# Kernel optimization log

Hardware: AMD Instinct MI355X
Metric: run time of the kernel (lower is better)

## Reference

```python
import jax, jax.numpy as jnp
import numpy as np

N = 100_000      # nodes
E = 1_600_000    # edges (avg degree 16)
D = 128          # emb_dim
L = 2            # num_layer
BN_EPS = 1e-5


def setup_inputs() -> dict:
    key = jax.random.key(0)
    ks = jax.random.split(key, 16)
    s = 0.05
    inp = {
        # int inputs
        "x": jax.random.randint(ks[0], (N, 9), 0, 2),
        "z": jax.random.randint(ks[1], (N,), 0, 1000),
        "edge_index": jax.random.randint(ks[2], (2, E), 0, N),
        "edge_attr": jax.random.randint(ks[3], (E, 3), 0, 2),
        # learned params
        "atom_emb": jax.random.normal(ks[4], (9, 119, D), jnp.float32) * s,  # padded stacked AtomEncoder tables
        "z_emb": jax.random.normal(ks[5], (1000, D), jnp.float32) * s,
        "bond_emb": jax.random.normal(ks[6], (L, 3, 6, D), jnp.float32) * s,  # padded BondEncoder tables per layer
        "eps": jnp.zeros((L,), jnp.float32),
        "W1": jax.random.normal(ks[7], (L, D, 2 * D), jnp.float32) * s,
        "b1": jnp.zeros((L, 2 * D), jnp.float32),
        "g1": jnp.ones((L, 2 * D), jnp.float32),
        "be1": jnp.zeros((L, 2 * D), jnp.float32),
        "W2": jax.random.normal(ks[8], (L, 2 * D, D), jnp.float32) * s,
        "b2": jnp.zeros((L, D), jnp.float32),
        "bng": jnp.ones((L, D), jnp.float32),
        "bnb": jnp.zeros((L, D), jnp.float32),
    }
    return inp


def _batchnorm(h, g, b):
    # training-mode BatchNorm1d: batch stats, biased variance
    m = h.mean(axis=0)
    v = h.var(axis=0)
    return (h - m) * jax.lax.rsqrt(v + BN_EPS) * g + b


def _multi_embed(tables, idx):
    # tables: [F, V, D], idx: [N, F] -> sum_f tables[f][idx[:, f]]  -> [N, D]
    return jax.vmap(lambda t, i: t[i], in_axes=(0, 1))(tables, idx).sum(axis=0)


def reference(x, z, edge_index, edge_attr, atom_emb, z_emb, bond_emb, eps,
              W1, b1, g1, be1, W2, b2, bng, bnb):
    src, dst = edge_index[0], edge_index[1]
    # h0 = AtomEncoder(x) + z_embedding(z)
    h = _multi_embed(atom_emb, x) + z_emb[z]
    for l in range(L):
        # GINConv: bond encode -> gather -> relu message -> scatter-add -> MLP
        e_emb = _multi_embed(bond_emb[l], edge_attr)          # [E, D]
        msg = jax.nn.relu(h[src] + e_emb)                      # [E, D]
        agg = jax.ops.segment_sum(msg, dst, num_segments=N)    # [N, D]
        pre = (1.0 + eps[l]) * h + agg
        hid = jax.nn.relu(_batchnorm(pre @ W1[l] + b1[l], g1[l], be1[l]))
        hconv = hid @ W2[l] + b2[l]
        h = _batchnorm(hconv, bng[l], bnb[l])
        if l < L - 1:
            h = jax.nn.relu(h)   # dropout ratio 0 -> identity
    return h
```

## Files before the change

kernel.cpp:

```cpp
#include <hip/hip_runtime.h>

#define D 128
#define BN_EPS 1e-5f
#define NSUB 1024
#define CAP2 2048

typedef __attribute__((ext_vector_type(8))) short short8;
typedef __attribute__((ext_vector_type(4))) float floatx4;

__device__ __forceinline__ float bf2f(unsigned short u) {
    unsigned int x = ((unsigned int)u) << 16;
    return __builtin_bit_cast(float, x);
}
__device__ __forceinline__ unsigned short f2bf(float f) {
    unsigned int x = __builtin_bit_cast(unsigned int, f);
    x = x + 0x7FFFu + ((x >> 16) & 1u);
    return (unsigned short)(x >> 16);
}
__device__ __forceinline__ int magdiv(unsigned int x, unsigned long long magic) {
    return (int)(((unsigned long long)x * magic) >> 44);
}

__global__ __launch_bounds__(256)
void setup_kernel(const int* __restrict__ x, const int* __restrict__ z,
                  const float* __restrict__ atom_emb, const float* __restrict__ z_emb,
                  unsigned short* __restrict__ hb, int N, int nbNode,
                  const float* __restrict__ bond_emb, float* __restrict__ comb,
                  const float* __restrict__ W1, unsigned short* __restrict__ w1p,
                  const float* __restrict__ W2, unsigned short* __restrict__ w2p) {
    const int b = blockIdx.x;
    const int tid = threadIdx.x;
    if (b < nbNode) {
        int gid = b * 256 + tid;
        int node = gid >> 5;
        if (node >= N) return;
        int d0 = (gid & 31) * 4;
        float4 acc = *(const float4*)(z_emb + (size_t)z[node] * D + d0);
#pragma unroll
        for (int f = 0; f < 9; ++f) {
            int v = x[node * 9 + f];
            const float4 t = *(const float4*)(atom_emb + (size_t)(f * 119 + v) * D + d0);
            acc.x += t.x; acc.y += t.y; acc.z += t.z; acc.w += t.w;
        }
        ushort4 o;
        o.x = f2bf(acc.x); o.y = f2bf(acc.y); o.z = f2bf(acc.z); o.w = f2bf(acc.w);
        *(ushort4*)(hb + (size_t)node * D + d0) = o;
    } else if (b < nbNode + 216) {
        int t = (b - nbNode) * 256 + tid;
        int layer = t / (216 * D);
        int idx = t - layer * (216 * D);
        int c = idx >> 7, d = idx & 127;
        int a0 = c / 36, a1 = (c / 6) % 6, a2 = c % 6;
        const float* bb = bond_emb + (size_t)layer * 3 * 6 * D;
        float v = bb[(0 * 6 + a0) * D + d] + bb[(1 * 6 + a1) * D + d] + bb[(2 * 6 + a2) * D + d];
        comb[(size_t)layer * 216 * D + idx] = v;
    } else {
        int isW2 = (b >= nbNode + 216 + 256);
        int t = (b - nbNode - 216 - (isW2 ? 256 : 0)) * 256 + tid;
        int layer = t >> 15;
        int idx = t & 32767;
        int logN = isW2 ? 7 : 8;
        int NCOLS = 1 << logN;
        int k = idx >> logN, n = idx & (NCOLS - 1);
        int k0 = k >> 5, kq = k & 31, q = kq >> 3, j = kq & 7;
        int tt = n >> 4, ln = n & 15;
        size_t dest = (((size_t)k0 * (NCOLS >> 4) + tt) << 9) + ((q << 4) + ln) * 8 + j;
        const float* W = (isW2 ? W2 : W1) + (size_t)layer * 32768;
        unsigned short* Wp = (isW2 ? w2p : w1p) + (size_t)layer * 32768;
        Wp[dest] = f2bf(W[idx]);
    }
}

__global__ __launch_bounds__(256)
void partition_kernel(const int* __restrict__ ei, const int* __restrict__ ea,
                      unsigned int* __restrict__ subL, int* __restrict__ tail2,
                      int E, int N, unsigned long long magic, int ntiles, int nblocks) {
    __shared__ int lcnt[1024], lbase[1024];
    const int tid = threadIdx.x;
    for (int tile = blockIdx.x; tile < ntiles; tile += nblocks) {
        const int tb = tile * 4096;
#pragma unroll
        for (int i = 0; i < 4; ++i) lcnt[tid + i * 256] = 0;
        __syncthreads();
        int sub[16];
        unsigned int entry[16];
#pragma unroll
        for (int j = 0; j < 16; ++j) {
            int e = tb + j * 256 + tid;
            if (e < E) {
                int dst = ei[E + e];
                int c = (ea[3 * e] * 6 + ea[3 * e + 1]) * 6 + ea[3 * e + 2];
                int k = magdiv((unsigned)dst * 1024u, magic);
                int lo = (int)(((long long)k * N + 1023) >> 10);
                sub[j] = k;
                entry[j] = (unsigned int)ei[e] | ((unsigned int)c << 17) |
                           ((unsigned int)(dst - lo) << 25);
                atomicAdd(&lcnt[k], 1);
            } else {
                sub[j] = -1;
            }
        }
        __syncthreads();
#pragma unroll
        for (int i = 0; i < 4; ++i) {
            int k = tid + i * 256;
            int c = lcnt[k];
            if (c) lbase[k] = atomicAdd(&tail2[k], c);
            lcnt[k] = 0;
        }
        __syncthreads();
#pragma unroll
        for (int j = 0; j < 16; ++j) {
            if (sub[j] >= 0) {
                int k = sub[j];
                int pos = lbase[k] + atomicAdd(&lcnt[k], 1);
                if (pos < CAP2) subL[(size_t)k * CAP2 + pos] = entry[j];
            }
        }
        __syncthreads();
    }
}

__global__ __launch_bounds__(1024)
void subscan_kernel(const int* __restrict__ tail2, int* __restrict__ subbase,
                    int* __restrict__ offsets, int N) {
    const int tid = threadIdx.x, lane = tid & 63, wid = tid >> 6;
    int v = min(tail2[tid], CAP2);
    int s = v;
#pragma unroll
    for (int off = 1; off < 64; off <<= 1) {
        int t = __shfl_up(s, off, 64);
        if (lane >= off) s += t;
    }
    __shared__ int ws[16];
    if (lane == 63) ws[wid] = s;
    __syncthreads();
    if (wid == 0) {
        int w = (lane < 16) ? ws[lane] : 0;
#pragma unroll
        for (int off = 1; off < 16; off <<= 1) {
            int t = __shfl_up(w, off, 64);
            if (lane >= off) w += t;
        }
        if (lane < 16) ws[lane] = w;
    }
    __syncthreads();
    int excl = (wid ? ws[wid - 1] : 0) + s - v;
    subbase[tid] = excl;
    if (tid == 1023) offsets[N] = excl + v;
}

__global__ __launch_bounds__(256)
void csr_sort_kernel(const unsigned int* __restrict__ subL, const int* __restrict__ tail2,
                     const int* __restrict__ subbase, int* __restrict__ offsets,
                     int* __restrict__ bucket, int N) {
    const int k = blockIdx.x;
    const int tid = threadIdx.x, lane = tid & 63, wid = tid >> 6;
    const int len = min(tail2[k], CAP2);
    const int base = subbase[k];
    const int lo = (int)(((long long)k * N + 1023) >> 10);
    const int hi = (int)(((long long)(k + 1) * N + 1023) >> 10);
    const int nn = hi - lo;
    __shared__ int cnt[128], loff[128], wsum[4];
    __shared__ unsigned int sorted[CAP2];
    const unsigned int* src = subL + (size_t)k * CAP2;

    if (tid < 128) cnt[tid] = 0;
    __syncthreads();
    for (int i = tid; i < len; i += 256) atomicAdd(&cnt[src[i] >> 25], 1);
    __syncthreads();
    int v = (tid < 128) ? cnt[tid] : 0;
    int s = v;
#pragma unroll
    for (int off = 1; off < 64; off <<= 1) {
        int t = __shfl_up(s, off, 64);
        if (lane >= off) s += t;
    }
    if (lane == 63) wsum[wid] = s;
    __syncthreads();
    if (tid < 128) loff[tid] = ((wid == 1) ? wsum[0] : 0) + s - v;
    __syncthreads();
    if (tid < nn) offsets[lo + tid] = base + loff[tid];
    if (tid < 128) cnt[tid] = 0;
    __syncthreads();
    for (int i = tid; i < len; i += 256) {
        unsigned int e = src[i];
        int ld = e >> 25;
        int pos = loff[ld] + atomicAdd(&cnt[ld], 1);
        sorted[pos] = e & 0x1FFFFFFu;
    }
    __syncthreads();
    for (int i = tid; i < len; i += 256) bucket[base + i] = (int)sorted[i];
}

__global__ __launch_bounds__(256)
void gather_reduce_kernel(const int* __restrict__ offsets, const int* __restrict__ bucket,
                          const float* __restrict__ comb,
                          const unsigned short* __restrict__ hb,
                          const float* __restrict__ eps_l,
                          unsigned short* __restrict__ pre, int N) {
    int gid = blockIdx.x * blockDim.x + threadIdx.x;
    int node = gid >> 4;
    if (node >= N) return;
    int d0 = (gid & 15) * 8;

    union U8 { int4 i; unsigned short u[8]; };
    union C8 { float4 v[2]; float f[8]; };
    float s = 1.0f + eps_l[0];
    float a[8];
    {
        U8 hv; hv.i = *(const int4*)(hb + (size_t)node * D + d0);
#pragma unroll
        for (int j = 0; j < 8; ++j) a[j] = bf2f(hv.u[j]) * s;
    }
    const int beg = offsets[node], end = offsets[node + 1];
    for (int p = beg; p < end; p += 4) {
        int rem = end - p;
        int pk0 = bucket[p];
        int pk1 = bucket[rem > 1 ? p + 1 : p];
        int pk2 = bucket[rem > 2 ? p + 2 : p];
        int pk3 = bucket[rem > 3 ? p + 3 : p];
        U8 h0, h1, h2, h3;
        C8 c0, c1, c2, c3;
        h0.i = *(const int4*)(hb + (size_t)(pk0 & 0x1FFFF) * D + d0);
        c0.v[0] = *(const float4*)(comb + (size_t)(pk0 >> 17) * D + d0);
        c0.v[1] = *(const float4*)(comb + (size_t)(pk0 >> 17) * D + d0 + 4);
        h1.i = *(const int4*)(hb + (size_t)(pk1 & 0x1FFFF) * D + d0);
        c1.v[0] = *(const float4*)(comb + (size_t)(pk1 >> 17) * D + d0);
        c1.v[1] = *(const float4*)(comb + (size_t)(pk1 >> 17) * D + d0 + 4);
        h2.i = *(const int4*)(hb + (size_t)(pk2 & 0x1FFFF) * D + d0);
        c2.v[0] = *(const float4*)(comb + (size_t)(pk2 >> 17) * D + d0);
        c2.v[1] = *(const float4*)(comb + (size_t)(pk2 >> 17) * D + d0 + 4);
        h3.i = *(const int4*)(hb + (size_t)(pk3 & 0x1FFFF) * D + d0);
        c3.v[0] = *(const float4*)(comb + (size_t)(pk3 >> 17) * D + d0);
        c3.v[1] = *(const float4*)(comb + (size_t)(pk3 >> 17) * D + d0 + 4);
#pragma unroll
        for (int j = 0; j < 8; ++j) a[j] += fmaxf(bf2f(h0.u[j]) + c0.f[j], 0.0f);
        if (rem > 1) {
#pragma unroll
            for (int j = 0; j < 8; ++j) a[j] += fmaxf(bf2f(h1.u[j]) + c1.f[j], 0.0f);
        }
        if (rem > 2) {
#pragma unroll
            for (int j = 0; j < 8; ++j) a[j] += fmaxf(bf2f(h2.u[j]) + c2.f[j], 0.0f);
        }
        if (rem > 3) {
#pragma unroll
            for (int j = 0; j < 8; ++j) a[j] += fmaxf(bf2f(h3.u[j]) + c3.f[j], 0.0f);
        }
    }
    U8 o;
#pragma unroll
    for (int j = 0; j < 8; ++j) o.u[j] = f2bf(a[j]);
    *(int4*)(pre + (size_t)node * D + d0) = o.i;
}

template <int K, int NCOLS, int TRANSFORM, int OUTBF>
__global__ __launch_bounds__(256)
void mfma_gemm_kernel(const unsigned short* __restrict__ A,
                      const unsigned short* __restrict__ Wp,
                      const float* __restrict__ bias,
                      const float* __restrict__ tscale, const float* __restrict__ tshift,
                      unsigned short* __restrict__ Cbf, float* __restrict__ Cf,
                      float* __restrict__ partial, int M) {
    constexpr int NT = NCOLS / 16;
    constexpr int NCHUNK = K / 32;
    constexpr int CPP = NCHUNK / 2;
    __shared__ unsigned short Ws[16384];
    __shared__ float red[NCOLS * 2];

    const int tid = threadIdx.x;
    const int wave = tid >> 6, lane = tid & 63;
    const int quad = lane >> 4, ln = lane & 15;
    const int m_base = blockIdx.x * 64 + wave * 16;
    int arow = m_base + ln;
    if (arow >= M) arow = M - 1;
    const int kq = quad * 8;

    int4 araw[NCHUNK];
#pragma unroll
    for (int c = 0; c < NCHUNK; ++c)
        araw[c] = *(const int4*)(A + (size_t)arow * K + c * 32 + kq);

    for (int i = tid; i < NCOLS * 2; i += 256) red[i] = 0.f;

    floatx4 acc[NT];
#pragma unroll
    for (int t = 0; t < NT; ++t) acc[t] = (floatx4){0.f, 0.f, 0.f, 0.f};

#pragma unroll
    for (int ph = 0; ph < 2; ++ph) {
        if (ph) __syncthreads();
#pragma unroll
        for (int i = 0; i < 16384; i += 2048)
            *(int4*)&Ws[i + tid * 8] = *(const int4*)&Wp[ph * 16384 + i + tid * 8];
        __syncthreads();
#pragma unroll
        for (int cc = 0; cc < CPP; ++cc) {
            const int c = ph * CPP + cc;
            short8 afrag;
            if constexpr (TRANSFORM) {
                union { int4 i; unsigned short u[8]; } raw;
                raw.i = araw[c];
                const int kb = c * 32 + kq;
                float4 sc0 = *(const float4*)(tscale + kb);
                float4 sc1 = *(const float4*)(tscale + kb + 4);
                float4 sh0 = *(const float4*)(tshift + kb);
                float4 sh1 = *(const float4*)(tshift + kb + 4);
                union { short8 v; unsigned short u[8]; } au;
                au.u[0] = f2bf(fmaxf(bf2f(raw.u[0]) * sc0.x + sh0.x, 0.f));
                au.u[1] = f2bf(fmaxf(bf2f(raw.u[1]) * sc0.y + sh0.y, 0.f));
                au.u[2] = f2bf(fmaxf(bf2f(raw.u[2]) * sc0.z + sh0.z, 0.f));
                au.u[3] = f2bf(fmaxf(bf2f(raw.u[3]) * sc0.w + sh0.w, 0.f));
                au.u[4] = f2bf(fmaxf(bf2f(raw.u[4]) * sc1.x + sh1.x, 0.f));
                au.u[5] = f2bf(fmaxf(bf2f(raw.u[5]) * sc1.y + sh1.y, 0.f));
                au.u[6] = f2bf(fmaxf(bf2f(raw.u[6]) * sc1.z + sh1.z, 0.f));
                au.u[7] = f2bf(fmaxf(bf2f(raw.u[7]) * sc1.w + sh1.w, 0.f));
                afrag = au.v;
            } else {
                afrag = __builtin_bit_cast(short8, araw[c]);
            }
#pragma unroll
            for (int t = 0; t < NT; ++t) {
                short8 bfrag = *(const short8*)&Ws[(((cc * NT) + t) << 9) + lane * 8];
                acc[t] = __builtin_amdgcn_mfma_f32_16x16x32_bf16(afrag, bfrag, acc[t], 0, 0, 0);
            }
        }
    }

#pragma unroll
    for (int t = 0; t < NT; ++t) {
        int col = t * 16 + ln;
        float bv = bias[col];
        float sv = 0.f, qv = 0.f;
#pragma unroll
        for (int r = 0; r < 4; ++r) {
            int row = m_base + quad * 4 + r;
            if (row < M) {
                float v = acc[t][r] + bv;
                sv += v; qv += v * v;
                if constexpr (OUTBF) Cbf[(size_t)row * NCOLS + col] = f2bf(v);
                else                 Cf[(size_t)row * NCOLS + col] = v;
            }
        }
        sv += __shfl_xor(sv, 16, 64); sv += __shfl_xor(sv, 32, 64);
        qv += __shfl_xor(qv, 16, 64); qv += __shfl_xor(qv, 32, 64);
        if (quad == 0) {
            atomicAdd(&red[col], sv);
            atomicAdd(&red[NCOLS + col], qv);
        }
    }
    __syncthreads();
    float* pout = partial + (size_t)blockIdx.x * (NCOLS * 2);
    for (int i = tid; i < NCOLS * 2; i += 256) pout[i] = red[i];
}

template <int NCOLS>
__global__ __launch_bounds__(256)
void reduce_stats_kernel(const float* __restrict__ partial, int nb,
                         const float* __restrict__ g, const float* __restrict__ b,
                         float* __restrict__ scale, float* __restrict__ shift, float invN) {
    const int col = blockIdx.x;
    const int tid = threadIdx.x;
    float s = 0.f, q = 0.f;
    for (int bb = tid; bb < nb; bb += 256) {
        const float* p = partial + (size_t)bb * (NCOLS * 2);
        s += p[col];
        q += p[NCOLS + col];
    }
#pragma unroll
    for (int off = 32; off > 0; off >>= 1) {
        s += __shfl_xor(s, off, 64);
        q += __shfl_xor(q, off, 64);
    }
    __shared__ float ws[4], wq[4];
    if ((tid & 63) == 0) { ws[tid >> 6] = s; wq[tid >> 6] = q; }
    __syncthreads();
    if (tid == 0) {
        s = ws[0] + ws[1] + ws[2] + ws[3];
        q = wq[0] + wq[1] + wq[2] + wq[3];
        float mean = s * invN;
        float var = q * invN - mean * mean;
        float inv = 1.0f / sqrtf(var + BN_EPS);
        float sc = g[col] * inv;
        scale[col] = sc;
        shift[col] = b[col] - mean * sc;
    }
}

__global__ void bn_apply_kernel(const unsigned short* __restrict__ Xb,
                                float* __restrict__ Yf, unsigned short* __restrict__ Yb,
                                const float* __restrict__ scale, const float* __restrict__ shift,
                                int N, int mode) {
    int gid = blockIdx.x * blockDim.x + threadIdx.x;
    int node = gid >> 5;
    if (node >= N) return;
    int d0 = (gid & 31) * 4;
    ushort4 b = *(const ushort4*)(Xb + (size_t)node * D + d0);
    float4 v;
    v.x = bf2f(b.x); v.y = bf2f(b.y); v.z = bf2f(b.z); v.w = bf2f(b.w);
    float4 sc = *(const float4*)(scale + d0);
    float4 sh = *(const float4*)(shift + d0);
    float4 o;
    o.x = v.x * sc.x + sh.x;
    o.y = v.y * sc.y + sh.y;
    o.z = v.z * sc.z + sh.z;
    o.w = v.w * sc.w + sh.w;
    if (mode == 0) {
        ushort4 ob;
        ob.x = f2bf(fmaxf(o.x, 0.f));
        ob.y = f2bf(fmaxf(o.y, 0.f));
        ob.z = f2bf(fmaxf(o.z, 0.f));
        ob.w = f2bf(fmaxf(o.w, 0.f));
        *(ushort4*)(Yb + (size_t)node * D + d0) = ob;
    } else {
        *(float4*)(Yf + (size_t)node * D + d0) = o;
    }
}

extern "C" void kernel_launch(void* const* d_in, const int* in_sizes, int n_in,
                              void* d_out, int out_size, void* d_ws, size_t ws_size,
                              hipStream_t stream) {
    const int*   x        = (const int*)d_in[0];
    const int*   z        = (const int*)d_in[1];
    const int*   ei       = (const int*)d_in[2];
    const int*   ea       = (const int*)d_in[3];
    const float* atom_emb = (const float*)d_in[4];
    const float* z_emb    = (const float*)d_in[5];
    const float* bond_emb = (const float*)d_in[6];
    const float* eps      = (const float*)d_in[7];
    const float* W1       = (const float*)d_in[8];
    const float* b1       = (const float*)d_in[9];
    const float* g1       = (const float*)d_in[10];
    const float* be1      = (const float*)d_in[11];
    const float* W2       = (const float*)d_in[12];
    const float* b2       = (const float*)d_in[13];
    const float* bng      = (const float*)d_in[14];
    const float* bnb      = (const float*)d_in[15];

    const int N = in_sizes[1];
    const int E = in_sizes[3] / 3;

    float* h = (float*)d_out;

    const int ngb = (N + 63) / 64;
    const unsigned long long magic = ((1ULL << 44) / (unsigned int)N) + 1;

    char* ws = (char*)d_ws;
    size_t off = 0;
    auto alloc = [&](size_t bytes) { void* p = ws + off; off += (bytes + 255) & ~(size_t)255; return p; };
    unsigned short* pre_bf = (unsigned short*)alloc((size_t)N * D * 2);
    unsigned short* out2_bf = pre_bf;
    unsigned short* out1_bf = (unsigned short*)alloc((size_t)N * 2 * D * 2);
    unsigned short* hb      = (unsigned short*)alloc((size_t)N * D * 2);
    int* offsets = (int*)alloc((size_t)(N + 1) * 4);
    int* bucket  = (int*)alloc((size_t)E * 4);
    unsigned int* subL = (unsigned int*)alloc((size_t)NSUB * CAP2 * 4);
    int* subbase = (int*)alloc(NSUB * 4);
    float* stats = (float*)alloc(1024 * 4);
    float* partial1 = (float*)alloc((size_t)ngb * 512 * 4);
    float* partial2 = (float*)alloc((size_t)ngb * 256 * 4);
    unsigned short* w1p  = (unsigned short*)alloc((size_t)2 * D * 2 * D * 2);
    unsigned short* w2p  = (unsigned short*)alloc((size_t)2 * 2 * D * D * 2);
    float* comb = (float*)alloc((size_t)2 * 216 * D * 4);
    int* tail2 = (int*)out1_bf;

    float* scale1 = stats;
    float* shift1 = stats + 256;
    float* scale2 = stats + 512;
    float* shift2 = stats + 640;

    const float invN = 1.0f / (float)N;
    const int ntiles = (E + 4095) / 4096;
    const int nbNode = (N * 32 + 255) / 256;

    hipMemsetAsync(tail2, 0, NSUB * sizeof(int), stream);
    partition_kernel<<<256, 256, 0, stream>>>(ei, ea, subL, tail2, E, N, magic, ntiles, 256);
    subscan_kernel<<<1, 1024, 0, stream>>>(tail2, subbase, offsets, N);
    csr_sort_kernel<<<NSUB, 256, 0, stream>>>(subL, tail2, subbase, offsets, bucket, N);

    setup_kernel<<<nbNode + 216 + 256 + 256, 256, 0, stream>>>(
        x, z, atom_emb, z_emb, hb, N, nbNode, bond_emb, comb, W1, w1p, W2, w2p);

    for (int l = 0; l < 2; ++l) {
        gather_reduce_kernel<<<(N * 16 + 255) / 256, 256, 0, stream>>>(
            offsets, bucket, comb + (size_t)l * 216 * D, hb, eps + l, pre_bf, N);

        mfma_gemm_kernel<128, 256, 0, 1><<<ngb, 256, 0, stream>>>(
            pre_bf, w1p + (size_t)l * D * 2 * D, b1 + (size_t)l * 2 * D,
            nullptr, nullptr, out1_bf, nullptr, partial1, N);
        reduce_stats_kernel<256><<<256, 256, 0, stream>>>(
            partial1, ngb, g1 + (size_t)l * 2 * D, be1 + (size_t)l * 2 * D,
            scale1, shift1, invN);

        mfma_gemm_kernel<256, 128, 1, 1><<<ngb, 256, 0, stream>>>(
            out1_bf, w2p + (size_t)l * 2 * D * D, b2 + (size_t)l * D,
            scale1, shift1, out2_bf, nullptr, partial2, N);
        reduce_stats_kernel<128><<<128, 256, 0, stream>>>(
            partial2, ngb, bng + (size_t)l * D, bnb + (size_t)l * D,
            scale2, shift2, invN);

        bn_apply_kernel<<<(N * 32 + 255) / 256, 256, 0, stream>>>(
            out2_bf, h, hb, scale2, shift2, N, l == 0 ? 0 : 1);
    }
}
```

Baseline: 537.9 us.

## Stage bf16 bond-combination table in LDS for gather-reduce

Stores the 216-entry combined bond embedding table in bf16 with a padded row stride. Each 1024-thread gather block copies its layer's table into shared memory and reads edge embeddings from LDS instead of global fp32. This removes the per-edge global reads of the combination rows and halves their width. In exchange every block pays a table copy and a barrier, the bond sums are rounded to bf16, and the larger blocks with higher LDS use may limit occupancy.

Measured after the change: 549.2 us. 2.1% more time.

```diff
diff --git a/kernel.cpp b/kernel.cpp
--- a/kernel.cpp
+++ b/kernel.cpp
@@ -4,6 +4,8 @@
 #define BN_EPS 1e-5f
 #define NSUB 1024
 #define CAP2 2048
+#define CSTRIDE 136
+#define CS_SHORTS (216 * CSTRIDE)
 
 typedef __attribute__((ext_vector_type(8))) short short8;
 typedef __attribute__((ext_vector_type(4))) float floatx4;
@@ -25,7 +27,7 @@
 void setup_kernel(const int* __restrict__ x, const int* __restrict__ z,
                   const float* __restrict__ atom_emb, const float* __restrict__ z_emb,
                   unsigned short* __restrict__ hb, int N, int nbNode,
-                  const float* __restrict__ bond_emb, float* __restrict__ comb,
+                  const float* __restrict__ bond_emb, unsigned short* __restrict__ comb,
                   const float* __restrict__ W1, unsigned short* __restrict__ w1p,
                   const float* __restrict__ W2, unsigned short* __restrict__ w2p) {
     const int b = blockIdx.x;
@@ -53,7 +55,7 @@
         int a0 = c / 36, a1 = (c / 6) % 6, a2 = c % 6;
         const float* bb = bond_emb + (size_t)layer * 3 * 6 * D;
         float v = bb[(0 * 6 + a0) * D + d] + bb[(1 * 6 + a1) * D + d] + bb[(2 * 6 + a2) * D + d];
-        comb[(size_t)layer * 216 * D + idx] = v;
+        comb[(size_t)layer * CS_SHORTS + c * CSTRIDE + d] = f2bf(v);
     } else {
         int isW2 = (b >= nbNode + 216 + 256);
         int t = (b - nbNode - 216 - (isW2 ? 256 : 0)) * 256 + tid;
@@ -193,19 +195,25 @@
     for (int i = tid; i < len; i += 256) bucket[base + i] = (int)sorted[i];
 }
 
-__global__ __launch_bounds__(256)
+__global__ __launch_bounds__(1024, 8)
 void gather_reduce_kernel(const int* __restrict__ offsets, const int* __restrict__ bucket,
-                          const float* __restrict__ comb,
+                          const unsigned short* __restrict__ combL,
                           const unsigned short* __restrict__ hb,
                           const float* __restrict__ eps_l,
                           unsigned short* __restrict__ pre, int N) {
-    int gid = blockIdx.x * blockDim.x + threadIdx.x;
-    int node = gid >> 4;
+    __shared__ unsigned short cs[CS_SHORTS];
+    {
+        const int4* srcv = (const int4*)combL;
+        int4* dstv = (int4*)cs;
+        for (int i = threadIdx.x; i < CS_SHORTS / 8; i += 1024) dstv[i] = srcv[i];
+    }
+    __syncthreads();
+
+    int node = blockIdx.x * 64 + (threadIdx.x >> 4);
     if (node >= N) return;
-    int d0 = (gid & 15) * 8;
+    int d0 = (threadIdx.x & 15) * 8;
 
     union U8 { int4 i; unsigned short u[8]; };
-    union C8 { float4 v[2]; float f[8]; };
     float s = 1.0f + eps_l[0];
     float a[8];
     {
@@ -220,33 +228,28 @@
         int pk1 = bucket[rem > 1 ? p + 1 : p];
         int pk2 = bucket[rem > 2 ? p + 2 : p];
         int pk3 = bucket[rem > 3 ? p + 3 : p];
-        U8 h0, h1, h2, h3;
-        C8 c0, c1, c2, c3;
+        U8 h0, h1, h2, h3, c0, c1, c2, c3;
         h0.i = *(const int4*)(hb + (size_t)(pk0 & 0x1FFFF) * D + d0);
-        c0.v[0] = *(const float4*)(comb + (size_t)(pk0 >> 17) * D + d0);
-        c0.v[1] = *(const float4*)(comb + (size_t)(pk0 >> 17) * D + d0 + 4);
         h1.i = *(const int4*)(hb + (size_t)(pk1 & 0x1FFFF) * D + d0);
-        c1.v[0] = *(const float4*)(comb + (size_t)(pk1 >> 17) * D + d0);
-        c1.v[1] = *(const float4*)(comb + (size_t)(pk1 >> 17) * D + d0 + 4);
         h2.i = *(const int4*)(hb + (size_t)(pk2 & 0x1FFFF) * D + d0);
-        c2.v[0] = *(const float4*)(comb + (size_t)(pk2 >> 17) * D + d0);
-        c2.v[1] = *(const float4*)(comb + (size_t)(pk2 >> 17) * D + d0 + 4);
         h3.i = *(const int4*)(hb + (size_t)(pk3 & 0x1FFFF) * D + d0);
-        c3.v[0] = *(const float4*)(comb + (size_t)(pk3 >> 17) * D + d0);
-        c3.v[1] = *(const float4*)(comb + (size_t)(pk3 >> 17) * D + d0 + 4);
-#pragma unroll
-        for (int j = 0; j < 8; ++j) a[j] += fmaxf(bf2f(h0.u[j]) + c0.f[j], 0.0f);
+        c0.i = *(const int4*)&cs[(pk0 >> 17) * CSTRIDE + d0];
+        c1.i = *(const int4*)&cs[(pk1 >> 17) * CSTRIDE + d0];
+        c2.i = *(const int4*)&cs[(pk2 >> 17) * CSTRIDE + d0];
+        c3.i = *(const int4*)&cs[(pk3 >> 17) * CSTRIDE + d0];
+#pragma unroll
+        for (int j = 0; j < 8; ++j) a[j] += fmaxf(bf2f(h0.u[j]) + bf2f(c0.u[j]), 0.0f);
         if (rem > 1) {
 #pragma unroll
-            for (int j = 0; j < 8; ++j) a[j] += fmaxf(bf2f(h1.u[j]) + c1.f[j], 0.0f);
+            for (int j = 0; j < 8; ++j) a[j] += fmaxf(bf2f(h1.u[j]) + bf2f(c1.u[j]), 0.0f);
         }
         if (rem > 2) {
 #pragma unroll
-            for (int j = 0; j < 8; ++j) a[j] += fmaxf(bf2f(h2.u[j]) + c2.f[j], 0.0f);
+            for (int j = 0; j < 8; ++j) a[j] += fmaxf(bf2f(h2.u[j]) + bf2f(c2.u[j]), 0.0f);
         }
         if (rem > 3) {
 #pragma unroll
-            for (int j = 0; j < 8; ++j) a[j] += fmaxf(bf2f(h3.u[j]) + c3.f[j], 0.0f);
+            for (int j = 0; j < 8; ++j) a[j] += fmaxf(bf2f(h3.u[j]) + bf2f(c3.u[j]), 0.0f);
         }
     }
     U8 o;
@@ -462,7 +465,7 @@
     float* partial2 = (float*)alloc((size_t)ngb * 256 * 4);
     unsigned short* w1p  = (unsigned short*)alloc((size_t)2 * D * 2 * D * 2);
     unsigned short* w2p  = (unsigned short*)alloc((size_t)2 * 2 * D * D * 2);
-    float* comb = (float*)alloc((size_t)2 * 216 * D * 4);
+    unsigned short* comb = (unsigned short*)alloc((size_t)2 * CS_SHORTS * 2);
     int* tail2 = (int*)out1_bf;
 
     float* scale1 = stats;
@@ -483,8 +486,8 @@
         x, z, atom_emb, z_emb, hb, N, nbNode, bond_emb, comb, W1, w1p, W2, w2p);
 
     for (int l = 0; l < 2; ++l) {
-        gather_reduce_kernel<<<(N * 16 + 255) / 256, 256, 0, stream>>>(
-            offsets, bucket, comb + (size_t)l * 216 * D, hb, eps + l, pre_bf, N);
+        gather_reduce_kernel<<<(N + 63) / 64, 1024, 0, stream>>>(
+            offsets, bucket, comb + (size_t)l * CS_SHORTS, hb, eps + l, pre_bf, N);
 
         mfma_gemm_kernel<128, 256, 0, 1><<<ngb, 256, 0, stream>>>(
             pre_bf, w1p + (size_t)l * D * 2 * D, b1 + (size_t)l * 2 * D,
```
